# Kernel tuning notes

Hardware: AMD Instinct MI355X
Metric: run time of the kernel (lower is better)

Reference implementation:

```python
import jax, jax.numpy as jnp
import numpy as np

VOCAB = 128
EMB = 16
HID = 512
B, T = 128, 1024


def setup_inputs() -> dict:
    key = jax.random.key(0)
    ks = jax.random.split(key, 8)
    s = 0.05
    return {
        "x": jax.random.randint(ks[0], (B, T), 0, VOCAB),
        "emb": jax.random.normal(ks[1], (VOCAB, EMB), jnp.float32) * s,
        "W_ih": jax.random.normal(ks[2], (HID, EMB), jnp.float32) * s,
        "W_hh": jax.random.normal(ks[3], (HID, HID), jnp.float32) * s,
        "b_ih": jax.random.normal(ks[4], (HID,), jnp.float32) * s,
        "b_hh": jax.random.normal(ks[5], (HID,), jnp.float32) * s,
        "W_fc": jax.random.normal(ks[6], (VOCAB, HID), jnp.float32) * s,
        "b_fc": jax.random.normal(ks[7], (VOCAB,), jnp.float32) * s,
    }


def reference(x, emb, W_ih, W_hh, b_ih, b_hh, W_fc, b_fc):
    # Embedding lookup: [B, T, EMB]
    xe = emb[x]
    # Precompute input-to-hidden part for all steps: [B, T, HID]
    xp = jnp.einsum('bte,he->bth', xe, W_ih) + b_ih + b_hh
    h0 = jnp.zeros((xe.shape[0], W_hh.shape[0]), xe.dtype)

    def step(h, xt):  # xt: [B, HID]
        h_new = jnp.tanh(xt + h @ W_hh.T)
        return h_new, h_new

    # scan over time: [T, B, HID]
    _, hs = jax.lax.scan(step, h0, jnp.swapaxes(xp, 0, 1))
    hs = jnp.swapaxes(hs, 0, 1)  # [B, T, HID]
    logits = jnp.einsum('bth,vh->btv', hs, W_fc) + b_fc  # [B, T, VOCAB]
    return logits
```

## Files before the change

kernel.cpp:

```cpp
#include <hip/hip_runtime.h>
#include <cstdint>


typedef short bf16x8 __attribute__((ext_vector_type(8)));
typedef float f32x4 __attribute__((ext_vector_type(4)));

#define VOCAB 128
#define EMB   16
#define HID   512
#define TT    1024
#define NCL   8
#define BB    16
#define JC    32
#define NWG   128
#define CLW   8192
#define BUFW  (NCL * CLW)
#define FLAGOFF (2 * BUFW)
#define PJC   33

__device__ __forceinline__ unsigned short f2bf(float f) {
  uint32_t u = __builtin_bit_cast(uint32_t, f);
  u += 0x7FFFu + ((u >> 16) & 1u);
  return (unsigned short)(u >> 16);
}
__device__ __forceinline__ float bf2f(unsigned short s) {
  uint32_t u = (uint32_t)s << 16;
  return __builtin_bit_cast(float, u);
}
__device__ __forceinline__ float ftanh(float z) {
  z = fminf(15.f, fmaxf(-15.f, z));
  float e = __expf(2.f * z);
  return (e - 1.f) * __builtin_amdgcn_rcpf(e + 1.f);
}
__device__ __forceinline__ uint32_t aload(const uint32_t* p) {
  return __hip_atomic_load(p, __ATOMIC_RELAXED, __HIP_MEMORY_SCOPE_AGENT);
}
__device__ __forceinline__ void astore(uint32_t* p, uint32_t v) {
  __hip_atomic_store(p, v, __ATOMIC_RELAXED, __HIP_MEMORY_SCOPE_AGENT);
}

__global__ __launch_bounds__(256, 1) void charrnn_kernel(
    const int* __restrict__ xin,
    const float* __restrict__ emb,
    const float* __restrict__ wih,
    const float* __restrict__ whh,
    const float* __restrict__ bih,
    const float* __restrict__ bhh,
    const float* __restrict__ wfc,
    const float* __restrict__ bfc,
    float* __restrict__ out,
    uint32_t* __restrict__ hx)
{
  __shared__ __align__(16) unsigned short a_hi[16 * 512];
  __shared__ __align__(16) unsigned short a_lo[16 * 512];
  __shared__ float ep[VOCAB * PJC];
  __shared__ unsigned char xtok[BB * TT];
  __shared__ __align__(16) float red[2][256];

  const int tid  = threadIdx.x;
  const int wave = tid >> 6;
  const int lane = tid & 63;
  const int col  = lane & 15;
  const int quad = lane >> 4;
  const int cl   = blockIdx.x & 7;
  const int m    = blockIdx.x >> 3;

  bf16x8 wfh[16], wfl[16], wfcf[8];
  if (wave < 2) {
    const int nrow = m * JC + wave * 16 + col;
    const float* wr = whh + (size_t)nrow * HID + quad * 8;
    #pragma unroll
    for (int ks = 0; ks < 16; ++ks) {
      bf16x8 hi, lo;
      #pragma unroll
      for (int j = 0; j < 8; ++j) {
        float w = wr[ks * 32 + j];
        unsigned short h = f2bf(w);
        hi[j] = (short)h;
        lo[j] = (short)f2bf(w - bf2f(h));
      }
      wfh[ks] = hi; wfl[ks] = lo;
    }
  } else {
    const int vrow = m * 8 + (col & 7);
    const float* wr = wfc + (size_t)vrow * HID + (wave - 2) * 256 + quad * 8;
    #pragma unroll
    for (int ks = 0; ks < 8; ++ks) {
      bf16x8 f;
      #pragma unroll
      for (int j = 0; j < 8; ++j) f[j] = (short)f2bf(wr[ks * 32 + j]);
      wfcf[ks] = f;
    }
  }
  const float bfcr = bfc[m * 8 + (col & 7)];

  for (int i = tid; i < 16 * 512; i += 256) { a_hi[i] = 0; a_lo[i] = 0; }
  for (int i = tid; i < VOCAB * JC; i += 256) {
    int v = i >> 5, jl = i & 31;
    int jg = m * JC + jl;
    float s = bih[jg] + bhh[jg];
    #pragma unroll
    for (int e = 0; e < EMB; ++e) s += emb[v * EMB + e] * wih[jg * EMB + e];
    ep[v * PJC + jl] = s;
  }
  for (int i = tid; i < BB * TT; i += 256) {
    int b = i >> 10, t = i & 1023;
    xtok[i] = (unsigned char)xin[(cl * BB + b) * TT + t];
  }
  __syncthreads();

  uint32_t* const flags = hx + FLAGOFF + cl * 32;
  f32x4 prev_lacc = {0.f, 0.f, 0.f, 0.f};

  #pragma unroll 1
  for (int t = 0; t <= TT + 1; ++t) {
    const int par = t & 1;

    if (wave >= 2 && t >= 2) {
      *(f32x4*)&red[wave - 2][lane * 4] = prev_lacc;
    }

    if (t >= 1 && t <= TT) {
      uint32_t f;
      do {
        f = aload(&flags[lane & 31]);
      } while (__all((int)(f >= (uint32_t)t)) == 0);
      asm volatile("" ::: "memory");

      const uint32_t* src = hx + par * BUFW + cl * CLW + tid;
      uint32_t v[32];
      #pragma unroll
      for (int i = 0; i < 32; ++i) v[i] = aload(src + 256 * i);
      #pragma unroll
      for (int i = 0; i < 16; ++i)
        *(uint32_t*)&a_hi[(tid + 256 * i) * 2] = v[i];
      #pragma unroll
      for (int i = 0; i < 16; ++i)
        *(uint32_t*)&a_lo[(tid + 256 * i) * 2] = v[16 + i];
    }
    __syncthreads();

    if (wave < 2) {
      if (t < TT) {
        f32x4 acc0 = {0.f,0.f,0.f,0.f}, acc1 = {0.f,0.f,0.f,0.f}, acc2 = {0.f,0.f,0.f,0.f};
        #pragma unroll
        for (int ks = 0; ks < 16; ++ks) {
          bf16x8 ah = *(const bf16x8*)&a_hi[ks * 512 + lane * 8];
          bf16x8 al = *(const bf16x8*)&a_lo[ks * 512 + lane * 8];
          acc0 = __builtin_amdgcn_mfma_f32_16x16x32_bf16(ah, wfh[ks], acc0, 0, 0, 0);
          acc1 = __builtin_amdgcn_mfma_f32_16x16x32_bf16(al, wfh[ks], acc1, 0, 0, 0);
          acc2 = __builtin_amdgcn_mfma_f32_16x16x32_bf16(ah, wfl[ks], acc2, 0, 0, 0);
        }
        const int jl = wave * 16 + col;
        uint32_t* wb = hx + ((t + 1) & 1) * BUFW + cl * CLW
                     + ((lane & 1) ? 4096 : 0)
                     + m * 256 + (wave * 2 + (col >> 3)) * 64 + ((col & 7) >> 1);
        #pragma unroll
        for (int i = 0; i < 4; ++i) {
          const int b = quad * 4 + i;
          float z = acc0[i] + acc1[i] + acc2[i]
                  + ep[(int)xtok[b * TT + t] * PJC + jl];
          float h = ftanh(z);
          unsigned short hi = f2bf(h);
          float lof = h - bf2f(hi);
          unsigned short lo = f2bf(lof);
          uint32_t pk = (uint32_t)hi | ((uint32_t)lo << 16);
          uint32_t pp = (uint32_t)__shfl_xor((int)pk, 1);
          uint32_t word = (lane & 1) ? ((pp >> 16) | (pk & 0xFFFF0000u))
                                     : ((pk & 0xFFFFu) | (pp << 16));
          astore(wb + b * 4, word);
        }
        asm volatile("s_waitcnt vmcnt(0)" ::: "memory");
        if (lane == 0) astore(&flags[m * 2 + wave], (uint32_t)(t + 1));
      }
    } else {
      if (wave == 2 && t >= 2 && col < 8) {
        #pragma unroll
        for (int i = 0; i < 4; ++i) {
          const int b = quad * 4 + i;
          float s = red[0][lane * 4 + i] + red[1][lane * 4 + i] + bfcr;
          out[((size_t)(cl * BB + b) * TT + (t - 2)) * VOCAB + m * 8 + col] = s;
        }
      }
      if (t >= 1 && t <= TT) {
        f32x4 lacc = {0.f, 0.f, 0.f, 0.f};
        const int kb = (wave - 2) * 8;
        #pragma unroll
        for (int ks = 0; ks < 8; ++ks) {
          bf16x8 ah = *(const bf16x8*)&a_hi[(kb + ks) * 512 + lane * 8];
          bf16x8 al = *(const bf16x8*)&a_lo[(kb + ks) * 512 + lane * 8];
          lacc = __builtin_amdgcn_mfma_f32_16x16x32_bf16(ah, wfcf[ks], lacc, 0, 0, 0);
          lacc = __builtin_amdgcn_mfma_f32_16x16x32_bf16(al, wfcf[ks], lacc, 0, 0, 0);
        }
        prev_lacc = lacc;
      }
    }
    __syncthreads();
  }
}

extern "C" void kernel_launch(void* const* d_in, const int* in_sizes, int n_in,
                              void* d_out, int out_size, void* d_ws, size_t ws_size,
                              hipStream_t stream) {
  (void)in_sizes; (void)n_in; (void)out_size;
  if (ws_size < (size_t)FLAGOFF * sizeof(uint32_t) + 4096) return;

  const int*   x    = (const int*)d_in[0];
  const float* embp = (const float*)d_in[1];
  const float* W_ih = (const float*)d_in[2];
  const float* W_hh = (const float*)d_in[3];
  const float* b_ih = (const float*)d_in[4];
  const float* b_hh = (const float*)d_in[5];
  const float* W_fc = (const float*)d_in[6];
  const float* b_fc = (const float*)d_in[7];

  hipMemsetAsync((uint32_t*)d_ws + FLAGOFF, 0, NCL * 32 * sizeof(uint32_t), stream);

  charrnn_kernel<<<NWG, 256, 0, stream>>>(x, embp, W_ih, W_hh, b_ih, b_hh, W_fc, b_fc,
                                          (float*)d_out, (uint32_t*)d_ws);
}
```

Baseline: 3.018 ms.

## Use XCD-local sc0 loads for flag polling and h exchange when cluster co-located

At startup each workgroup records its XCC_ID and checks whether all 16 workgroups in its cluster sit on the same XCD. If they do, flag polling and the per-step hidden-state loads use raw global_load_dword with only sc0, which keeps coherence at the shared L2 instead of going device-wide, so the per-step exchange latency should drop. If the cluster spans XCDs, or polling exceeds a spin bound, the code falls back to the original agent-scope atomics. The risks are the reliance on how blocks map to XCDs and on L2 coherence semantics for sc0 loads.

Result: slower. 8.215 ms (+172.2%).

```diff
diff --git a/kernel.cpp b/kernel.cpp
--- a/kernel.cpp
+++ b/kernel.cpp
@@ -16,6 +16,7 @@
 #define CLW   8192
 #define BUFW  (NCL * CLW)
 #define FLAGOFF (2 * BUFW)
+#define XCDOFF  (FLAGOFF + NCL * 32)
 #define PJC   33
 
 __device__ __forceinline__ unsigned short f2bf(float f) {
@@ -56,6 +57,8 @@
   __shared__ float ep[VOCAB * PJC];
   __shared__ unsigned char xtok[BB * TT];
   __shared__ __align__(16) float red[2][256];
+  __shared__ uint32_t s_xcd[16];
+  __shared__ int s_fastf;
 
   const int tid  = threadIdx.x;
   const int wave = tid >> 6;
@@ -107,10 +110,30 @@
     int b = i >> 10, t = i & 1023;
     xtok[i] = (unsigned char)xin[(cl * BB + b) * TT + t];
   }
+
+  uint32_t myxcd;
+  asm volatile("s_getreg_b32 %0, hwreg(HW_REG_XCC_ID)" : "=s"(myxcd));
+  myxcd &= 0xFFu;
+  if (tid == 0) astore(hx + XCDOFF + blockIdx.x, myxcd + 1u);
+  if (tid < 16) {
+    uint32_t v;
+    do { v = aload(hx + XCDOFF + tid * 8 + cl); } while (v == 0u);
+    s_xcd[tid] = v;
+  }
   __syncthreads();
+  if (tid == 0) {
+    int ok = 1;
+    #pragma unroll
+    for (int i = 1; i < 16; ++i) ok &= (s_xcd[i] == s_xcd[0]);
+    s_fastf = ok;
+  }
+  __syncthreads();
+  const bool fastmap = (s_fastf != 0);
 
   uint32_t* const flags = hx + FLAGOFF + cl * 32;
+  const uint32_t* const fp = flags + (lane & 31);
   f32x4 prev_lacc = {0.f, 0.f, 0.f, 0.f};
+  bool deg = !fastmap;
 
   #pragma unroll 1
   for (int t = 0; t <= TT + 1; ++t) {
@@ -121,16 +144,42 @@
     }
 
     if (t >= 1 && t <= TT) {
-      uint32_t f;
-      do {
-        f = aload(&flags[lane & 31]);
-      } while (__all((int)(f >= (uint32_t)t)) == 0);
+      bool seen = false;
+      if (!deg) {
+        for (int s = 0; s < 65536 && !seen; ++s) {
+          uint32_t f;
+          asm volatile("global_load_dword %0, %1, off sc0\n\t"
+                       "s_waitcnt vmcnt(0)"
+                       : "=&v"(f) : "v"(fp) : "memory");
+          seen = __all((int)(f >= (uint32_t)t)) != 0;
+        }
+        if (!seen) deg = true;
+      }
+      if (!seen) {
+        uint32_t f;
+        do { f = aload(fp); } while (__all((int)(f >= (uint32_t)t)) == 0);
+      }
       asm volatile("" ::: "memory");
 
       const uint32_t* src = hx + par * BUFW + cl * CLW + tid;
       uint32_t v[32];
-      #pragma unroll
-      for (int i = 0; i < 32; ++i) v[i] = aload(src + 256 * i);
+      if (!deg) {
+        #pragma unroll
+        for (int g = 0; g < 8; ++g) {
+          asm volatile("global_load_dword %0, %4, off sc0\n\t"
+                       "global_load_dword %1, %4, off offset:1024 sc0\n\t"
+                       "global_load_dword %2, %4, off offset:2048 sc0\n\t"
+                       "global_load_dword %3, %4, off offset:3072 sc0"
+                       : "=&v"(v[4 * g]), "=&v"(v[4 * g + 1]),
+                         "=&v"(v[4 * g + 2]), "=&v"(v[4 * g + 3])
+                       : "v"(src + g * 1024));
+        }
+        asm volatile("s_waitcnt vmcnt(0)" ::: "memory");
+        __builtin_amdgcn_sched_barrier(0);
+      } else {
+        #pragma unroll
+        for (int i = 0; i < 32; ++i) v[i] = aload(src + 256 * i);
+      }
       #pragma unroll
       for (int i = 0; i < 16; ++i)
         *(uint32_t*)&a_hi[(tid + 256 * i) * 2] = v[i];
@@ -214,7 +263,8 @@
   const float* W_fc = (const float*)d_in[6];
   const float* b_fc = (const float*)d_in[7];
 
-  hipMemsetAsync((uint32_t*)d_ws + FLAGOFF, 0, NCL * 32 * sizeof(uint32_t), stream);
+  hipMemsetAsync((uint32_t*)d_ws + FLAGOFF, 0,
+                 (NCL * 32 + NWG) * sizeof(uint32_t), stream);
 
   charrnn_kernel<<<NWG, 256, 0, stream>>>(x, embp, W_ih, W_hh, b_ih, b_hh, W_fc, b_fc,
                                           (float*)d_out, (uint32_t*)d_ws);
```

## Embed step tags in exchanged hidden-state words to skip flag polling

Applied to the files above, without the earlier changes.

Each hidden value is now exchanged as a 21-bit fixed-point number packed with an 11-bit step tag. Readers load the exchange buffer directly and check the tags, and fall back to flag polling only when some tag is stale. This removes the flag round-trip and the vmcnt wait from the critical inter-workgroup synchronisation path. The cost is lower hidden-state precision (about 2^-20 quantisation instead of the hi/lo bf16 split) and bf16 hi/lo reconstruction work on the read side.

Result: slower. 3.459 ms (+14.6%).

```diff
diff --git a/kernel.cpp b/kernel.cpp
--- a/kernel.cpp
+++ b/kernel.cpp
@@ -57,6 +57,9 @@
   __shared__ unsigned char xtok[BB * TT];
   __shared__ __align__(16) float red[2][256];
 
+  uint32_t* const a_hi32 = (uint32_t*)a_hi;
+  uint32_t* const a_lo32 = (uint32_t*)a_lo;
+
   const int tid  = threadIdx.x;
   const int wave = tid >> 6;
   const int lane = tid & 63;
@@ -109,7 +112,16 @@
   }
   __syncthreads();
 
+  const int jl = wave * 16 + col;
+  const int C0 = m * 512 + ((wave * 2 + (col >> 3)) << 7) + (col & 7);
+  const float rcp20 = 1.f / 1048576.f;
+  const uint32_t hsel = 0xFFFF0000u;
+  uint32_t* const dbase = (tid & 1) ? a_lo32 : a_hi32;
+  const uint32_t psel = (tid & 1) ? 0x03020706u : 0x05040100u;
+  const int dword0 = tid >> 1;
+
   uint32_t* const flags = hx + FLAGOFF + cl * 32;
+  const uint32_t* const fp = flags + (lane & 31);
   f32x4 prev_lacc = {0.f, 0.f, 0.f, 0.f};
 
   #pragma unroll 1
@@ -121,22 +133,39 @@
     }
 
     if (t >= 1 && t <= TT) {
-      uint32_t f;
-      do {
-        f = aload(&flags[lane & 31]);
-      } while (__all((int)(f >= (uint32_t)t)) == 0);
-      asm volatile("" ::: "memory");
-
+      const uint32_t tag = (uint32_t)t & 0x7FFu;
       const uint32_t* src = hx + par * BUFW + cl * CLW + tid;
       uint32_t v[32];
       #pragma unroll
       for (int i = 0; i < 32; ++i) v[i] = aload(src + 256 * i);
-      #pragma unroll
-      for (int i = 0; i < 16; ++i)
-        *(uint32_t*)&a_hi[(tid + 256 * i) * 2] = v[i];
-      #pragma unroll
-      for (int i = 0; i < 16; ++i)
-        *(uint32_t*)&a_lo[(tid + 256 * i) * 2] = v[16 + i];
+      uint32_t bad = 0;
+      #pragma unroll
+      for (int i = 0; i < 32; ++i) bad |= v[i] ^ tag;
+      bad &= 0x7FFu;
+      if (__any((int)bad)) {
+        uint32_t f;
+        do { f = aload(fp); } while (__all((int)(f >= (uint32_t)t)) == 0);
+        for (;;) {
+          #pragma unroll
+          for (int i = 0; i < 32; ++i) v[i] = aload(src + 256 * i);
+          bad = 0;
+          #pragma unroll
+          for (int i = 0; i < 32; ++i) bad |= v[i] ^ tag;
+          bad &= 0x7FFu;
+          if (__any((int)bad) == 0) break;
+        }
+      }
+      #pragma unroll
+      for (int i = 0; i < 32; ++i) {
+        float h = (float)(((int)v[i]) >> 11) * rcp20;
+        uint32_t uh = __builtin_bit_cast(uint32_t, h) & hsel;
+        float l = h - __builtin_bit_cast(float, uh);
+        uint32_t pk = __builtin_amdgcn_perm(__builtin_bit_cast(uint32_t, l),
+                                            uh, 0x07060302u);
+        uint32_t pp = (uint32_t)__shfl_xor((int)pk, 1);
+        uint32_t wd = __builtin_amdgcn_perm(pp, pk, psel);
+        dbase[128 * i + dword0] = wd;
+      }
     }
     __syncthreads();
 
@@ -151,26 +180,19 @@
           acc1 = __builtin_amdgcn_mfma_f32_16x16x32_bf16(al, wfh[ks], acc1, 0, 0, 0);
           acc2 = __builtin_amdgcn_mfma_f32_16x16x32_bf16(ah, wfl[ks], acc2, 0, 0, 0);
         }
-        const int jl = wave * 16 + col;
-        uint32_t* wb = hx + ((t + 1) & 1) * BUFW + cl * CLW
-                     + ((lane & 1) ? 4096 : 0)
-                     + m * 256 + (wave * 2 + (col >> 3)) * 64 + ((col & 7) >> 1);
+        const uint32_t ntag = (uint32_t)(t + 1) & 0x7FFu;
+        uint32_t* wb = hx + ((t + 1) & 1) * BUFW + cl * CLW + C0;
         #pragma unroll
         for (int i = 0; i < 4; ++i) {
           const int b = quad * 4 + i;
           float z = acc0[i] + acc1[i] + acc2[i]
                   + ep[(int)xtok[b * TT + t] * PJC + jl];
           float h = ftanh(z);
-          unsigned short hi = f2bf(h);
-          float lof = h - bf2f(hi);
-          unsigned short lo = f2bf(lof);
-          uint32_t pk = (uint32_t)hi | ((uint32_t)lo << 16);
-          uint32_t pp = (uint32_t)__shfl_xor((int)pk, 1);
-          uint32_t word = (lane & 1) ? ((pp >> 16) | (pk & 0xFFFF0000u))
-                                     : ((pk & 0xFFFFu) | (pp << 16));
-          astore(wb + b * 4, word);
-        }
-        asm volatile("s_waitcnt vmcnt(0)" ::: "memory");
+          int q = __float2int_rn(h * 1048576.f);
+          q = max(min(q, 1048575), -1048576);
+          astore(wb + b * 8, ((uint32_t)q << 11) | ntag);
+        }
+        asm volatile("" ::: "memory");
         if (lane == 0) astore(&flags[m * 2 + wave], (uint32_t)(t + 1));
       }
     } else {
```
